# Kernel tuning notes

Hardware: AMD Instinct MI355X
Metric: run time of the kernel (lower is better)

## Reference

```python
import jax, jax.numpy as jnp
import numpy as np

N_NODES = 50000


def _gcn_conv(x, W, b, src, dst, n):
    # PyG GCNConv: h = x @ W, symmetric-normalized aggregation, then + bias.
    h = x @ W  # [N, out]
    deg = jax.ops.segment_sum(jnp.ones_like(dst, dtype=h.dtype), dst, num_segments=n)
    dinv = jnp.where(deg > 0, jax.lax.rsqrt(jnp.maximum(deg, 1e-12)), 0.0)
    norm = dinv[src] * dinv[dst]  # [E]
    msg = h[src] * norm[:, None]  # gather + scale, [E, out]
    out = jax.ops.segment_sum(msg, dst, num_segments=n)
    return out + b


def setup_inputs() -> dict:
    key = jax.random.key(0)
    ks = jax.random.split(key, 8)
    d_in, d_h, d_out = 256, 256, 128
    E = 800000
    x = jax.random.normal(ks[0], (N_NODES, d_in), dtype=jnp.float32)
    edge_index = jax.random.randint(ks[1], (2, E), 0, N_NODES, dtype=jnp.int64)
    def glorot(k, shape):
        lim = np.sqrt(6.0 / (shape[0] + shape[1]))
        return jax.random.uniform(k, shape, jnp.float32, -lim, lim)
    return {
        "x": x,
        "edge_index": edge_index,
        "W1": glorot(ks[2], (d_in, d_h)), "b1": jnp.zeros((d_h,), jnp.float32),
        "W2": glorot(ks[3], (d_h, d_h)), "b2": jnp.zeros((d_h,), jnp.float32),
        "W3": glorot(ks[4], (d_h, d_out)), "b3": jnp.zeros((d_out,), jnp.float32),
    }


def reference(x, edge_index, W1, b1, W2, b2, W3, b3):
    n = x.shape[0]
    # add self-loops once (PyG GCNConv default add_self_loops=True)
    loop = jnp.arange(n, dtype=edge_index.dtype)
    src = jnp.concatenate([edge_index[0], loop])
    dst = jnp.concatenate([edge_index[1], loop])
    h = _gcn_conv(x, W1, b1, src, dst, n)
    h = jax.nn.relu(h)  # dropout is identity in eval mode
    h = _gcn_conv(h, W2, b2, src, dst, n)
    h = jax.nn.relu(h)
    h = _gcn_conv(h, W3, b3, src, dst, n)
    return h
```

## Files before the change

### kernel.cpp

```cpp
#include <hip/hip_runtime.h>
#include <stdint.h>

typedef short v8s __attribute__((ext_vector_type(8)));
typedef float v4f __attribute__((ext_vector_type(4)));
typedef float v2f __attribute__((ext_vector_type(2)));

__device__ inline float bf2f(unsigned short h) {
    union { unsigned u; float f; } c; c.u = ((unsigned)h) << 16; return c.f;
}
__device__ inline unsigned short f2bf(float f) {
    union { float f; unsigned u; } c; c.f = f;
    unsigned u = c.u;
    unsigned r = (u + 0x7FFFu + ((u >> 16) & 1u)) >> 16;
    return (unsigned short)r;
}
__device__ inline void gl_lds16(const unsigned short* g, unsigned short* l) {
    __builtin_amdgcn_global_load_lds(
        (const __attribute__((address_space(1))) unsigned int*)(g),
        (__attribute__((address_space(3))) unsigned int*)(l), 16, 0, 0);
}

__global__ void k_pre1(const int* __restrict__ dst, int E,
                       int* __restrict__ cnt, int* __restrict__ seq,
                       const float* __restrict__ x, unsigned short* __restrict__ A,
                       int n, int mpad,
                       const float* __restrict__ W1, const float* __restrict__ W2,
                       const float* __restrict__ W3, unsigned short* __restrict__ Wt,
                       int gE, int gX) {
    int b = blockIdx.x;
    if (b < gE) {
        int e = b * 256 + threadIdx.x;
        if (e < E) seq[e] = atomicAdd(&cnt[dst[e]], 1);
    } else if (b < gE + gX) {
        int g = (b - gE) * 256 + threadIdx.x;
        int total = mpad * 64;
        if (g >= total) return;
        int row = g >> 6;
        float4 v;
        if (row < n) v = ((const float4*)x)[(size_t)g];
        else v = make_float4(0.f, 0.f, 0.f, 0.f);
        ushort4 o;
        o.x = f2bf(v.x); o.y = f2bf(v.y); o.z = f2bf(v.z); o.w = f2bf(v.w);
        ((ushort4*)A)[(size_t)g] = o;
    } else {
        int idx = (b - gE - gX) * 256 + threadIdx.x;
        const float* W; int base, N;
        if (idx < 65536)       { W = W1; base = 0;      N = 256; }
        else if (idx < 131072) { W = W2; base = 65536;  N = 256; }
        else                   { W = W3; base = 131072; N = 128; }
        int loc = idx - base;
        int nn = loc >> 8;
        int k = loc & 255;
        Wt[idx] = f2bf(W[(size_t)k * N + nn]);
    }
}

__global__ void k_scan1(const int* __restrict__ cnt, int n, int* __restrict__ incl,
                        int* __restrict__ bsum) {
    __shared__ int sm[256];
    int t = threadIdx.x;
    int i = blockIdx.x * 256 + t;
    int v = (i < n) ? cnt[i] : 0;
    sm[t] = v; __syncthreads();
    for (int off = 1; off < 256; off <<= 1) {
        int add = (t >= off) ? sm[t - off] : 0;
        __syncthreads();
        sm[t] += add;
        __syncthreads();
    }
    if (i < n) incl[i] = sm[t];
    if (t == 255) bsum[blockIdx.x] = sm[255];
}

__global__ void k_scan2(const int* __restrict__ bsum, int nb, int* __restrict__ boff) {
    __shared__ int sm[256];
    int t = threadIdx.x;
    int v = (t < nb) ? bsum[t] : 0;
    sm[t] = v; __syncthreads();
    for (int off = 1; off < 256; off <<= 1) {
        int add = (t >= off) ? sm[t - off] : 0;
        __syncthreads();
        sm[t] += add;
        __syncthreads();
    }
    if (t < nb) boff[t] = sm[t] - v;
}

__global__ void k_scan3(const int* __restrict__ cnt, int n, const int* __restrict__ boff,
                        int* __restrict__ rs, float* __restrict__ dinv) {
    int i = blockIdx.x * 256 + threadIdx.x;
    if (i < n) {
        int c = cnt[i];
        rs[i] = rs[i] + boff[blockIdx.x] - c;
        dinv[i] = rsqrtf((float)(c + 1));
    }
}

__global__ void k_scatter2(const int* __restrict__ src, const int* __restrict__ dst,
                           const int* __restrict__ seq, int E,
                           const int* __restrict__ rs, int* __restrict__ col) {
    int e = blockIdx.x * 256 + threadIdx.x;
    if (e < E) col[rs[dst[e]] + seq[e]] = src[e];
}

__launch_bounds__(256, 4)
__global__ void k_gemm(const unsigned short* __restrict__ A,
                       const unsigned short* __restrict__ Wt,
                       unsigned short* __restrict__ Hs,
                       const float* __restrict__ dinv, int n, int N) {
    __shared__ unsigned short sA[128 * 32];
    __shared__ unsigned short sB[128 * 32];
    const int t = threadIdx.x;
    const int lane = t & 63;
    const int wave = t >> 6;
    const int wm = wave >> 1, wn = wave & 1;
    const int m0 = blockIdx.x * 128;
    const int n0 = blockIdx.y * 128;

    v4f acc[4][4];
#pragma unroll
    for (int i = 0; i < 4; i++)
#pragma unroll
        for (int j = 0; j < 4; j++)
#pragma unroll
            for (int r = 0; r < 4; r++) acc[i][j][r] = 0.f;

    const int c0 = t, c1 = t + 256;
    const int r0 = c0 >> 2, kc0 = (c0 & 3) * 8;
    const int r1 = c1 >> 2, kc1 = (c1 & 3) * 8;
    const size_t aBase0 = (size_t)(m0 + r0) * 256 + kc0;
    const size_t aBase1 = (size_t)(m0 + r1) * 256 + kc1;
    const size_t bBase0 = (size_t)(n0 + r0) * 256 + kc0;
    const size_t bBase1 = (size_t)(n0 + r1) * 256 + kc1;

    const int q = lane >> 4;
    const int lm = lane & 15;

    for (int k0 = 0; k0 < 256; k0 += 32) {
        __syncthreads();
        gl_lds16(A + aBase0 + k0, &sA[c0 * 8]);
        gl_lds16(A + aBase1 + k0, &sA[c1 * 8]);
        gl_lds16(Wt + bBase0 + k0, &sB[c0 * 8]);
        gl_lds16(Wt + bBase1 + k0, &sB[c1 * 8]);
        __syncthreads();

        v8s afr[4], bfr[4];
#pragma unroll
        for (int i = 0; i < 4; i++) {
            int r = wm * 64 + i * 16 + lm;
            afr[i] = *(const v8s*)&sA[r * 32 + q * 8];
        }
#pragma unroll
        for (int j = 0; j < 4; j++) {
            int nn = wn * 64 + j * 16 + lm;
            bfr[j] = *(const v8s*)&sB[nn * 32 + q * 8];
        }
#pragma unroll
        for (int i = 0; i < 4; i++)
#pragma unroll
            for (int j = 0; j < 4; j++)
                acc[i][j] = __builtin_amdgcn_mfma_f32_16x16x32_bf16(afr[i], bfr[j],
                                                                    acc[i][j], 0, 0, 0);
    }

#pragma unroll
    for (int i = 0; i < 4; i++) {
        int mbase = m0 + wm * 64 + i * 16 + q * 4;
#pragma unroll
        for (int r = 0; r < 4; r++) {
            int m = mbase + r;
            float s = (m < n) ? dinv[m] : 0.f;
#pragma unroll
            for (int j = 0; j < 4; j++) {
                int colI = n0 + wn * 64 + j * 16 + lm;
                Hs[(size_t)m * N + colI] = f2bf(acc[i][j][r] * s);
            }
        }
    }
}

template <int D, bool RELU, bool F32OUT>
__launch_bounds__(256, 8)
__global__ void k_agg(const unsigned short* __restrict__ Hs,
                      const int* __restrict__ rs, const int* __restrict__ cnt,
                      const int* __restrict__ col, const float* __restrict__ dinv,
                      const float* __restrict__ bias,
                      unsigned short* __restrict__ outb, float* __restrict__ outf,
                      int n, int nzero) {
    constexpr int LPN = D / 8;
    constexpr int NPG = 64 / LPN;
    const int lane = threadIdx.x & 63;
    const int i = blockIdx.x * 4 + (threadIdx.x >> 6);
    if (i >= n) return;
    const int g = lane / LPN;
    const int cl = lane % LPN;

    v2f acc[4];
#pragma unroll
    for (int k = 0; k < 4; k++) acc[k] = (v2f){0.f, 0.f};

    auto accq = [&](unsigned u, int k) {
        union { unsigned uu; float f; } lo, hi;
        lo.uu = u << 16;
        hi.uu = u & 0xffff0000u;
        v2f t; t[0] = lo.f; t[1] = hi.f;
        acc[k] += t;
    };
    auto acc16 = [&](uint4 q) { accq(q.x, 0); accq(q.y, 1); accq(q.z, 2); accq(q.w, 3); };

    const unsigned short* base = Hs + cl * 8;
    const int s = rs[i], deg = cnt[i];
    const int T = deg + 1;
    const int Tpad = (T + NPG - 1) & ~(NPG - 1);

    for (int b = 0; b < Tpad; b += 64) {
        int t = b + lane;
        int v;
        if (t == 0) v = i;
        else if (t <= deg) v = col[s + t - 1];
        else v = nzero;
        int lim = min(64, Tpad - b);
        int t2 = 0;
        for (; t2 + 4 * NPG <= lim; t2 += 4 * NPG) {
            int c0 = __shfl(v, t2 + 0 * NPG + g);
            int c1 = __shfl(v, t2 + 1 * NPG + g);
            int c2 = __shfl(v, t2 + 2 * NPG + g);
            int c3 = __shfl(v, t2 + 3 * NPG + g);
            uint4 q0 = *(const uint4*)(base + (size_t)c0 * D);
            uint4 q1 = *(const uint4*)(base + (size_t)c1 * D);
            uint4 q2 = *(const uint4*)(base + (size_t)c2 * D);
            uint4 q3 = *(const uint4*)(base + (size_t)c3 * D);
            acc16(q0); acc16(q1); acc16(q2); acc16(q3);
        }
        for (; t2 + NPG <= lim; t2 += NPG) {
            int c0 = __shfl(v, t2 + g);
            uint4 q0 = *(const uint4*)(base + (size_t)c0 * D);
            acc16(q0);
        }
    }

#pragma unroll
    for (int off = LPN; off < 64; off <<= 1) {
#pragma unroll
        for (int k = 0; k < 4; k++) {
            acc[k][0] += __shfl_xor(acc[k][0], off);
            acc[k][1] += __shfl_xor(acc[k][1], off);
        }
    }

    if (g == 0) {
        float di = dinv[i];
        float o[8];
#pragma unroll
        for (int k = 0; k < 4; k++) {
            o[2 * k + 0] = di * acc[k][0] + bias[cl * 8 + 2 * k + 0];
            o[2 * k + 1] = di * acc[k][1] + bias[cl * 8 + 2 * k + 1];
        }
        if (RELU) {
#pragma unroll
            for (int k = 0; k < 8; k++) o[k] = fmaxf(o[k], 0.f);
        }
        if constexpr (F32OUT) {
            float* p = outf + (size_t)i * D + cl * 8;
            *(float4*)p = make_float4(o[0], o[1], o[2], o[3]);
            *(float4*)(p + 4) = make_float4(o[4], o[5], o[6], o[7]);
        } else {
            uint4 q;
            q.x = ((unsigned)f2bf(o[1]) << 16) | f2bf(o[0]);
            q.y = ((unsigned)f2bf(o[3]) << 16) | f2bf(o[2]);
            q.z = ((unsigned)f2bf(o[5]) << 16) | f2bf(o[4]);
            q.w = ((unsigned)f2bf(o[7]) << 16) | f2bf(o[6]);
            *(uint4*)(outb + (size_t)i * D + cl * 8) = q;
        }
    }
}

extern "C" void kernel_launch(void* const* d_in, const int* in_sizes, int n_in,
                              void* d_out, int out_size, void* d_ws, size_t ws_size,
                              hipStream_t stream) {
    const float* x  = (const float*)d_in[0];
    const int*   ei = (const int*)d_in[1];
    const float* W1 = (const float*)d_in[2];
    const float* b1 = (const float*)d_in[3];
    const float* W2 = (const float*)d_in[4];
    const float* b2 = (const float*)d_in[5];
    const float* W3 = (const float*)d_in[6];
    const float* b3 = (const float*)d_in[7];

    const int n = in_sizes[0] / 256;
    const int E = in_sizes[1] / 2;
    const int mpad = ((n + 127) / 128) * 128;

    char* ws = (char*)d_ws;
    size_t off = 0;
    auto alloc = [&](size_t bytes) -> void* {
        void* p = ws + off;
        off += (bytes + 255) & ~(size_t)255;
        return p;
    };
    int* cnt      = (int*)alloc((size_t)n * 4);
    int* rs       = (int*)alloc((size_t)n * 4);
    float* dinv   = (float*)alloc((size_t)n * 4);
    int* bsum     = (int*)alloc(256 * 4);
    int* boff     = (int*)alloc(256 * 4);
    int* seq      = (int*)alloc((size_t)E * 4);
    int* col      = (int*)alloc((size_t)E * 4);
    unsigned short* Wt = (unsigned short*)alloc((size_t)163840 * 2);
    unsigned short* W1t = Wt;
    unsigned short* W2t = Wt + 65536;
    unsigned short* W3t = Wt + 131072;
    unsigned short* bufA = (unsigned short*)alloc((size_t)mpad * 256 * 2);
    unsigned short* bufB = (unsigned short*)alloc((size_t)mpad * 256 * 2);
    (void)ws_size; (void)n_in; (void)out_size;

    const int* srcp = ei;
    const int* dstp = ei + E;
    const int gE = (E + 255) / 256;
    const int gN = (n + 255) / 256;
    const int gX = (mpad * 64 + 255) / 256;
    const int gW = 640;

    hipMemsetAsync(cnt, 0, (size_t)n * 4, stream);

    k_pre1<<<gE + gX + gW, 256, 0, stream>>>(dstp, E, cnt, seq, x, bufA, n, mpad,
                                             W1, W2, W3, Wt, gE, gX);
    k_scan1<<<gN, 256, 0, stream>>>(cnt, n, rs, bsum);
    k_scan2<<<1, 256, 0, stream>>>(bsum, gN, boff);
    k_scan3<<<gN, 256, 0, stream>>>(cnt, n, boff, rs, dinv);
    k_scatter2<<<gE, 256, 0, stream>>>(srcp, dstp, seq, E, rs, col);

    const int gAgg = (n + 3) / 4;
    dim3 gg1(mpad / 128, 2);
    k_gemm<<<gg1, 256, 0, stream>>>(bufA, W1t, bufB, dinv, n, 256);
    k_agg<256, true, false><<<gAgg, 256, 0, stream>>>(bufB, rs, cnt, col, dinv, b1,
                                                      bufA, nullptr, n, n);
    k_gemm<<<gg1, 256, 0, stream>>>(bufA, W2t, bufB, dinv, n, 256);
    k_agg<256, true, false><<<gAgg, 256, 0, stream>>>(bufB, rs, cnt, col, dinv, b2,
                                                      bufA, nullptr, n, n);
    dim3 gg3(mpad / 128, 1);
    k_gemm<<<gg3, 256, 0, stream>>>(bufA, W3t, bufB, dinv, n, 128);
    k_agg<128, false, true><<<gAgg, 256, 0, stream>>>(bufB, rs, cnt, col, dinv, b3,
                                                      nullptr, (float*)d_out, n, n);
}
```

Baseline: 354.9 us.

## Double-buffer GEMM LDS tiles and fuse scan stages two and three

The GEMM now keeps two LDS buffers per operand and prefetches the next K-slice while MFMAs run on the current one, with a single barrier per iteration instead of two. Launch bounds drop from 4 to 3 blocks per CU to allow for the doubled shared memory. Separately, the single-block block-offset scan and the apply kernel are merged: each block sums the preceding block totals itself, which removes one launch. Correctness of the one-barrier double buffer depends on the async global-to-LDS loads being complete before the next barrier, and the reduced occupancy could offset some of the overlap gain.

```diff
diff --git a/kernel.cpp b/kernel.cpp
--- a/kernel.cpp
+++ b/kernel.cpp
@@ -72,26 +72,23 @@
     if (t == 255) bsum[blockIdx.x] = sm[255];
 }
 
-__global__ void k_scan2(const int* __restrict__ bsum, int nb, int* __restrict__ boff) {
-    __shared__ int sm[256];
+__global__ void k_scan23(const int* __restrict__ cnt, int n,
+                         const int* __restrict__ bsum,
+                         int* __restrict__ rs, float* __restrict__ dinv) {
+    __shared__ int red[256];
     int t = threadIdx.x;
-    int v = (t < nb) ? bsum[t] : 0;
-    sm[t] = v; __syncthreads();
-    for (int off = 1; off < 256; off <<= 1) {
-        int add = (t >= off) ? sm[t - off] : 0;
+    int acc = 0;
+    for (int j = t; j < (int)blockIdx.x; j += 256) acc += bsum[j];
+    red[t] = acc; __syncthreads();
+    for (int s = 128; s > 0; s >>= 1) {
+        if (t < s) red[t] += red[t + s];
         __syncthreads();
-        sm[t] += add;
-        __syncthreads();
-    }
-    if (t < nb) boff[t] = sm[t] - v;
-}
-
-__global__ void k_scan3(const int* __restrict__ cnt, int n, const int* __restrict__ boff,
-                        int* __restrict__ rs, float* __restrict__ dinv) {
-    int i = blockIdx.x * 256 + threadIdx.x;
+    }
+    int boff = red[0];
+    int i = blockIdx.x * 256 + t;
     if (i < n) {
         int c = cnt[i];
-        rs[i] = rs[i] + boff[blockIdx.x] - c;
+        rs[i] = rs[i] + boff - c;
         dinv[i] = rsqrtf((float)(c + 1));
     }
 }
@@ -103,13 +100,13 @@
     if (e < E) col[rs[dst[e]] + seq[e]] = src[e];
 }
 
-__launch_bounds__(256, 4)
+__launch_bounds__(256, 3)
 __global__ void k_gemm(const unsigned short* __restrict__ A,
                        const unsigned short* __restrict__ Wt,
                        unsigned short* __restrict__ Hs,
                        const float* __restrict__ dinv, int n, int N) {
-    __shared__ unsigned short sA[128 * 32];
-    __shared__ unsigned short sB[128 * 32];
+    __shared__ unsigned short sA[2][128 * 32];
+    __shared__ unsigned short sB[2][128 * 32];
     const int t = threadIdx.x;
     const int lane = t & 63;
     const int wave = t >> 6;
@@ -136,24 +133,32 @@
     const int q = lane >> 4;
     const int lm = lane & 15;
 
+    gl_lds16(A + aBase0, &sA[0][c0 * 8]);
+    gl_lds16(A + aBase1, &sA[0][c1 * 8]);
+    gl_lds16(Wt + bBase0, &sB[0][c0 * 8]);
+    gl_lds16(Wt + bBase1, &sB[0][c1 * 8]);
+
     for (int k0 = 0; k0 < 256; k0 += 32) {
+        const int cur = (k0 >> 5) & 1;
         __syncthreads();
-        gl_lds16(A + aBase0 + k0, &sA[c0 * 8]);
-        gl_lds16(A + aBase1 + k0, &sA[c1 * 8]);
-        gl_lds16(Wt + bBase0 + k0, &sB[c0 * 8]);
-        gl_lds16(Wt + bBase1 + k0, &sB[c1 * 8]);
-        __syncthreads();
+        if (k0 < 224) {
+            const int nxt = cur ^ 1;
+            gl_lds16(A + aBase0 + k0 + 32, &sA[nxt][c0 * 8]);
+            gl_lds16(A + aBase1 + k0 + 32, &sA[nxt][c1 * 8]);
+            gl_lds16(Wt + bBase0 + k0 + 32, &sB[nxt][c0 * 8]);
+            gl_lds16(Wt + bBase1 + k0 + 32, &sB[nxt][c1 * 8]);
+        }
 
         v8s afr[4], bfr[4];
 #pragma unroll
         for (int i = 0; i < 4; i++) {
             int r = wm * 64 + i * 16 + lm;
-            afr[i] = *(const v8s*)&sA[r * 32 + q * 8];
+            afr[i] = *(const v8s*)&sA[cur][r * 32 + q * 8];
         }
 #pragma unroll
         for (int j = 0; j < 4; j++) {
             int nn = wn * 64 + j * 16 + lm;
-            bfr[j] = *(const v8s*)&sB[nn * 32 + q * 8];
+            bfr[j] = *(const v8s*)&sB[cur][nn * 32 + q * 8];
         }
 #pragma unroll
         for (int i = 0; i < 4; i++)
@@ -302,7 +307,6 @@
     int* rs       = (int*)alloc((size_t)n * 4);
     float* dinv   = (float*)alloc((size_t)n * 4);
     int* bsum     = (int*)alloc(256 * 4);
-    int* boff     = (int*)alloc(256 * 4);
     int* seq      = (int*)alloc((size_t)E * 4);
     int* col      = (int*)alloc((size_t)E * 4);
     unsigned short* Wt = (unsigned short*)alloc((size_t)163840 * 2);
@@ -325,8 +329,7 @@
     k_pre1<<<gE + gX + gW, 256, 0, stream>>>(dstp, E, cnt, seq, x, bufA, n, mpad,
                                              W1, W2, W3, Wt, gE, gX);
     k_scan1<<<gN, 256, 0, stream>>>(cnt, n, rs, bsum);
-    k_scan2<<<1, 256, 0, stream>>>(bsum, gN, boff);
-    k_scan3<<<gN, 256, 0, stream>>>(cnt, n, boff, rs, dinv);
+    k_scan23<<<gN, 256, 0, stream>>>(cnt, n, bsum, rs, dinv);
     k_scatter2<<<gE, 256, 0, stream>>>(srcp, dstp, seq, E, rs, col);
 
     const int gAgg = (n + 3) / 4;
```

Result: slower. 364.3 us (+2.6%).

## Merge scan into one kernel and fuse edge scatter with first GEMM launch

Applied to the files above, without the earlier changes.

Replaces the three-kernel prefix scan with a single kernel in which each block recomputes its prefix by reducing all preceding counts. The CSR column scatter is merged into the first GEMM launch as extra blocks, so the two independent pieces of work run concurrently. Together this removes three kernel launches and their serialization gaps. In exchange, each scan block redundantly reads up to n counts, which is quadratic-ish work but small at this size, and the scatter blocks share a launch with the GEMM's register and LDS budget.

```diff
diff --git a/kernel.cpp b/kernel.cpp
--- a/kernel.cpp
+++ b/kernel.cpp
@@ -55,52 +55,108 @@
     }
 }
 
-__global__ void k_scan1(const int* __restrict__ cnt, int n, int* __restrict__ incl,
-                        int* __restrict__ bsum) {
+__global__ void k_scan(const int* __restrict__ cnt, int n,
+                       int* __restrict__ rs, float* __restrict__ dinv) {
     __shared__ int sm[256];
-    int t = threadIdx.x;
-    int i = blockIdx.x * 256 + t;
-    int v = (i < n) ? cnt[i] : 0;
+    __shared__ int preS;
+    const int t = threadIdx.x;
+    const int base = blockIdx.x * 256;
+
+    int acc = 0;
+    for (int j = t; j < base; j += 256) acc += cnt[j];
+    sm[t] = acc; __syncthreads();
+    for (int s = 128; s > 0; s >>= 1) {
+        if (t < s) sm[t] += sm[t + s];
+        __syncthreads();
+    }
+    if (t == 0) preS = sm[0];
+    __syncthreads();
+
+    const int i = base + t;
+    const int v = (i < n) ? cnt[i] : 0;
     sm[t] = v; __syncthreads();
     for (int off = 1; off < 256; off <<= 1) {
-        int add = (t >= off) ? sm[t - off] : 0;
-        __syncthreads();
-        sm[t] += add;
-        __syncthreads();
-    }
-    if (i < n) incl[i] = sm[t];
-    if (t == 255) bsum[blockIdx.x] = sm[255];
-}
-
-__global__ void k_scan2(const int* __restrict__ bsum, int nb, int* __restrict__ boff) {
-    __shared__ int sm[256];
-    int t = threadIdx.x;
-    int v = (t < nb) ? bsum[t] : 0;
-    sm[t] = v; __syncthreads();
-    for (int off = 1; off < 256; off <<= 1) {
-        int add = (t >= off) ? sm[t - off] : 0;
-        __syncthreads();
-        sm[t] += add;
-        __syncthreads();
-    }
-    if (t < nb) boff[t] = sm[t] - v;
-}
-
-__global__ void k_scan3(const int* __restrict__ cnt, int n, const int* __restrict__ boff,
-                        int* __restrict__ rs, float* __restrict__ dinv) {
-    int i = blockIdx.x * 256 + threadIdx.x;
+        int a = (t >= off) ? sm[t - off] : 0;
+        __syncthreads();
+        sm[t] += a;
+        __syncthreads();
+    }
     if (i < n) {
-        int c = cnt[i];
-        rs[i] = rs[i] + boff[blockIdx.x] - c;
-        dinv[i] = rsqrtf((float)(c + 1));
-    }
-}
-
-__global__ void k_scatter2(const int* __restrict__ src, const int* __restrict__ dst,
-                           const int* __restrict__ seq, int E,
-                           const int* __restrict__ rs, int* __restrict__ col) {
-    int e = blockIdx.x * 256 + threadIdx.x;
-    if (e < E) col[rs[dst[e]] + seq[e]] = src[e];
+        rs[i] = preS + sm[t] - v;
+        dinv[i] = rsqrtf((float)(v + 1));
+    }
+}
+
+__device__ __forceinline__ void gemm_body(
+        const unsigned short* __restrict__ A, const unsigned short* __restrict__ Wt,
+        unsigned short* __restrict__ Hs, const float* __restrict__ dinv,
+        int n, int N, int m0, int n0,
+        unsigned short* sA, unsigned short* sB) {
+    const int t = threadIdx.x;
+    const int lane = t & 63;
+    const int wave = t >> 6;
+    const int wm = wave >> 1, wn = wave & 1;
+
+    v4f acc[4][4];
+#pragma unroll
+    for (int i = 0; i < 4; i++)
+#pragma unroll
+        for (int j = 0; j < 4; j++)
+#pragma unroll
+            for (int r = 0; r < 4; r++) acc[i][j][r] = 0.f;
+
+    const int c0 = t, c1 = t + 256;
+    const int r0 = c0 >> 2, kc0 = (c0 & 3) * 8;
+    const int r1 = c1 >> 2, kc1 = (c1 & 3) * 8;
+    const size_t aBase0 = (size_t)(m0 + r0) * 256 + kc0;
+    const size_t aBase1 = (size_t)(m0 + r1) * 256 + kc1;
+    const size_t bBase0 = (size_t)(n0 + r0) * 256 + kc0;
+    const size_t bBase1 = (size_t)(n0 + r1) * 256 + kc1;
+
+    const int q = lane >> 4;
+    const int lm = lane & 15;
+
+    for (int k0 = 0; k0 < 256; k0 += 32) {
+        __syncthreads();
+        gl_lds16(A + aBase0 + k0, &sA[c0 * 8]);
+        gl_lds16(A + aBase1 + k0, &sA[c1 * 8]);
+        gl_lds16(Wt + bBase0 + k0, &sB[c0 * 8]);
+        gl_lds16(Wt + bBase1 + k0, &sB[c1 * 8]);
+        __syncthreads();
+
+        v8s afr[4], bfr[4];
+#pragma unroll
+        for (int i = 0; i < 4; i++) {
+            int r = wm * 64 + i * 16 + lm;
+            afr[i] = *(const v8s*)&sA[r * 32 + q * 8];
+        }
+#pragma unroll
+        for (int j = 0; j < 4; j++) {
+            int nn = wn * 64 + j * 16 + lm;
+            bfr[j] = *(const v8s*)&sB[nn * 32 + q * 8];
+        }
+#pragma unroll
+        for (int i = 0; i < 4; i++)
+#pragma unroll
+            for (int j = 0; j < 4; j++)
+                acc[i][j] = __builtin_amdgcn_mfma_f32_16x16x32_bf16(afr[i], bfr[j],
+                                                                    acc[i][j], 0, 0, 0);
+    }
+
+#pragma unroll
+    for (int i = 0; i < 4; i++) {
+        int mbase = m0 + wm * 64 + i * 16 + q * 4;
+#pragma unroll
+        for (int r = 0; r < 4; r++) {
+            int m = mbase + r;
+            float s = (m < n) ? dinv[m] : 0.f;
+#pragma unroll
+            for (int j = 0; j < 4; j++) {
+                int colI = n0 + wn * 64 + j * 16 + lm;
+                Hs[(size_t)m * N + colI] = f2bf(acc[i][j][r] * s);
+            }
+        }
+    }
 }
 
 __launch_bounds__(256, 4)
@@ -110,73 +166,28 @@
                        const float* __restrict__ dinv, int n, int N) {
     __shared__ unsigned short sA[128 * 32];
     __shared__ unsigned short sB[128 * 32];
-    const int t = threadIdx.x;
-    const int lane = t & 63;
-    const int wave = t >> 6;
-    const int wm = wave >> 1, wn = wave & 1;
-    const int m0 = blockIdx.x * 128;
-    const int n0 = blockIdx.y * 128;
-
-    v4f acc[4][4];
-#pragma unroll
-    for (int i = 0; i < 4; i++)
-#pragma unroll
-        for (int j = 0; j < 4; j++)
-#pragma unroll
-            for (int r = 0; r < 4; r++) acc[i][j][r] = 0.f;
-
-    const int c0 = t, c1 = t + 256;
-    const int r0 = c0 >> 2, kc0 = (c0 & 3) * 8;
-    const int r1 = c1 >> 2, kc1 = (c1 & 3) * 8;
-    const size_t aBase0 = (size_t)(m0 + r0) * 256 + kc0;
-    const size_t aBase1 = (size_t)(m0 + r1) * 256 + kc1;
-    const size_t bBase0 = (size_t)(n0 + r0) * 256 + kc0;
-    const size_t bBase1 = (size_t)(n0 + r1) * 256 + kc1;
-
-    const int q = lane >> 4;
-    const int lm = lane & 15;
-
-    for (int k0 = 0; k0 < 256; k0 += 32) {
-        __syncthreads();
-        gl_lds16(A + aBase0 + k0, &sA[c0 * 8]);
-        gl_lds16(A + aBase1 + k0, &sA[c1 * 8]);
-        gl_lds16(Wt + bBase0 + k0, &sB[c0 * 8]);
-        gl_lds16(Wt + bBase1 + k0, &sB[c1 * 8]);
-        __syncthreads();
-
-        v8s afr[4], bfr[4];
-#pragma unroll
-        for (int i = 0; i < 4; i++) {
-            int r = wm * 64 + i * 16 + lm;
-            afr[i] = *(const v8s*)&sA[r * 32 + q * 8];
-        }
-#pragma unroll
-        for (int j = 0; j < 4; j++) {
-            int nn = wn * 64 + j * 16 + lm;
-            bfr[j] = *(const v8s*)&sB[nn * 32 + q * 8];
-        }
-#pragma unroll
-        for (int i = 0; i < 4; i++)
-#pragma unroll
-            for (int j = 0; j < 4; j++)
-                acc[i][j] = __builtin_amdgcn_mfma_f32_16x16x32_bf16(afr[i], bfr[j],
-                                                                    acc[i][j], 0, 0, 0);
-    }
-
-#pragma unroll
-    for (int i = 0; i < 4; i++) {
-        int mbase = m0 + wm * 64 + i * 16 + q * 4;
-#pragma unroll
-        for (int r = 0; r < 4; r++) {
-            int m = mbase + r;
-            float s = (m < n) ? dinv[m] : 0.f;
-#pragma unroll
-            for (int j = 0; j < 4; j++) {
-                int colI = n0 + wn * 64 + j * 16 + lm;
-                Hs[(size_t)m * N + colI] = f2bf(acc[i][j][r] * s);
-            }
-        }
-    }
+    gemm_body(A, Wt, Hs, dinv, n, N, blockIdx.x * 128, blockIdx.y * 128, sA, sB);
+}
+
+__launch_bounds__(256, 4)
+__global__ void k_sg(const unsigned short* __restrict__ A,
+                     const unsigned short* __restrict__ Wt,
+                     unsigned short* __restrict__ Hs,
+                     const float* __restrict__ dinv, int n, int N, int nmb,
+                     const int* __restrict__ src, const int* __restrict__ dst,
+                     const int* __restrict__ seq, int E,
+                     const int* __restrict__ rs, int* __restrict__ col,
+                     int gemmBlocks) {
+    __shared__ unsigned short sA[128 * 32];
+    __shared__ unsigned short sB[128 * 32];
+    const int b = blockIdx.x;
+    if (b >= gemmBlocks) {
+        int e = (b - gemmBlocks) * 256 + threadIdx.x;
+        if (e < E) col[rs[dst[e]] + seq[e]] = src[e];
+        return;
+    }
+    const int bx = b % nmb, by = b / nmb;
+    gemm_body(A, Wt, Hs, dinv, n, N, bx * 128, by * 128, sA, sB);
 }
 
 template <int D, bool RELU, bool F32OUT>
@@ -295,14 +306,12 @@
     size_t off = 0;
     auto alloc = [&](size_t bytes) -> void* {
         void* p = ws + off;
-        off += (bytes + 255) & ~(size_t)255;
+        off += (bytes + 511) & ~(size_t)511;
         return p;
     };
     int* cnt      = (int*)alloc((size_t)n * 4);
     int* rs       = (int*)alloc((size_t)n * 4);
     float* dinv   = (float*)alloc((size_t)n * 4);
-    int* bsum     = (int*)alloc(256 * 4);
-    int* boff     = (int*)alloc(256 * 4);
     int* seq      = (int*)alloc((size_t)E * 4);
     int* col      = (int*)alloc((size_t)E * 4);
     unsigned short* Wt = (unsigned short*)alloc((size_t)163840 * 2);
@@ -319,25 +328,26 @@
     const int gN = (n + 255) / 256;
     const int gX = (mpad * 64 + 255) / 256;
     const int gW = 640;
+    const int nmb = mpad / 128;
 
     hipMemsetAsync(cnt, 0, (size_t)n * 4, stream);
 
     k_pre1<<<gE + gX + gW, 256, 0, stream>>>(dstp, E, cnt, seq, x, bufA, n, mpad,
                                              W1, W2, W3, Wt, gE, gX);
-    k_scan1<<<gN, 256, 0, stream>>>(cnt, n, rs, bsum);
-    k_scan2<<<1, 256, 0, stream>>>(bsum, gN, boff);
-    k_scan3<<<gN, 256, 0, stream>>>(cnt, n, boff, rs, dinv);
-    k_scatter2<<<gE, 256, 0, stream>>>(srcp, dstp, seq, E, rs, col);
+    k_scan<<<gN, 256, 0, stream>>>(cnt, n, rs, dinv);
+
+    const int gemmBlocks = nmb * 2;
+    k_sg<<<gemmBlocks + gE, 256, 0, stream>>>(bufA, W1t, bufB, dinv, n, 256, nmb,
+                                              srcp, dstp, seq, E, rs, col, gemmBlocks);
 
     const int gAgg = (n + 3) / 4;
-    dim3 gg1(mpad / 128, 2);
-    k_gemm<<<gg1, 256, 0, stream>>>(bufA, W1t, bufB, dinv, n, 256);
     k_agg<256, true, false><<<gAgg, 256, 0, stream>>>(bufB, rs, cnt, col, dinv, b1,
                                                       bufA, nullptr, n, n);
-    k_gemm<<<gg1, 256, 0, stream>>>(bufA, W2t, bufB, dinv, n, 256);
+    dim3 gg2(nmb, 2);
+    k_gemm<<<gg2, 256, 0, stream>>>(bufA, W2t, bufB, dinv, n, 256);
     k_agg<256, true, false><<<gAgg, 256, 0, stream>>>(bufB, rs, cnt, col, dinv, b2,
                                                       bufA, nullptr, n, n);
-    dim3 gg3(mpad / 128, 1);
+    dim3 gg3(nmb, 1);
     k_gemm<<<gg3, 256, 0, stream>>>(bufA, W3t, bufB, dinv, n, 128);
     k_agg<128, false, true><<<gAgg, 256, 0, stream>>>(bufB, rs, cnt, col, dinv, b3,
                                                       nullptr, (float*)d_out, n, n);
```

After: 381.2 us. 1.07x slower.

## Fuse x bf16 conversion into first GEMM and merge scan kernels

Applied to the files above, without the earlier changes.

Removes the separate fp32-to-bf16 conversion of x from the preprocessing kernel and adds a k_gemm_x variant that loads fp32 x directly, converts in registers and writes into LDS, so the bf16 copy of x is never written or re-read. It also fuses the block-offset scan and finalize kernels into one, where each block reduces the preceding block sums itself, saving one launch. In exchange, the first GEMM uses plain register loads instead of direct global-to-LDS loads and reads x once per column tile (twice in total). The pre-kernel is no longer slowed by the conversion work.

```diff
diff --git a/kernel.cpp b/kernel.cpp
--- a/kernel.cpp
+++ b/kernel.cpp
@@ -22,28 +22,15 @@
 
 __global__ void k_pre1(const int* __restrict__ dst, int E,
                        int* __restrict__ cnt, int* __restrict__ seq,
-                       const float* __restrict__ x, unsigned short* __restrict__ A,
-                       int n, int mpad,
                        const float* __restrict__ W1, const float* __restrict__ W2,
                        const float* __restrict__ W3, unsigned short* __restrict__ Wt,
-                       int gE, int gX) {
+                       int gE) {
     int b = blockIdx.x;
     if (b < gE) {
         int e = b * 256 + threadIdx.x;
         if (e < E) seq[e] = atomicAdd(&cnt[dst[e]], 1);
-    } else if (b < gE + gX) {
-        int g = (b - gE) * 256 + threadIdx.x;
-        int total = mpad * 64;
-        if (g >= total) return;
-        int row = g >> 6;
-        float4 v;
-        if (row < n) v = ((const float4*)x)[(size_t)g];
-        else v = make_float4(0.f, 0.f, 0.f, 0.f);
-        ushort4 o;
-        o.x = f2bf(v.x); o.y = f2bf(v.y); o.z = f2bf(v.z); o.w = f2bf(v.w);
-        ((ushort4*)A)[(size_t)g] = o;
     } else {
-        int idx = (b - gE - gX) * 256 + threadIdx.x;
+        int idx = (b - gE) * 256 + threadIdx.x;
         const float* W; int base, N;
         if (idx < 65536)       { W = W1; base = 0;      N = 256; }
         else if (idx < 131072) { W = W2; base = 65536;  N = 256; }
@@ -72,26 +59,23 @@
     if (t == 255) bsum[blockIdx.x] = sm[255];
 }
 
-__global__ void k_scan2(const int* __restrict__ bsum, int nb, int* __restrict__ boff) {
-    __shared__ int sm[256];
+__global__ void k_scan23(const int* __restrict__ cnt, int n,
+                         const int* __restrict__ bsum,
+                         int* __restrict__ rs, float* __restrict__ dinv) {
+    __shared__ int red[256];
     int t = threadIdx.x;
-    int v = (t < nb) ? bsum[t] : 0;
-    sm[t] = v; __syncthreads();
-    for (int off = 1; off < 256; off <<= 1) {
-        int add = (t >= off) ? sm[t - off] : 0;
-        __syncthreads();
-        sm[t] += add;
-        __syncthreads();
-    }
-    if (t < nb) boff[t] = sm[t] - v;
-}
-
-__global__ void k_scan3(const int* __restrict__ cnt, int n, const int* __restrict__ boff,
-                        int* __restrict__ rs, float* __restrict__ dinv) {
-    int i = blockIdx.x * 256 + threadIdx.x;
+    int acc = 0;
+    for (int j = t; j < (int)blockIdx.x; j += 256) acc += bsum[j];
+    red[t] = acc; __syncthreads();
+    for (int s = 128; s > 0; s >>= 1) {
+        if (t < s) red[t] += red[t + s];
+        __syncthreads();
+    }
+    int boff = red[0];
+    int i = blockIdx.x * 256 + t;
     if (i < n) {
         int c = cnt[i];
-        rs[i] = rs[i] + boff[blockIdx.x] - c;
+        rs[i] = rs[i] + boff - c;
         dinv[i] = rsqrtf((float)(c + 1));
     }
 }
@@ -142,6 +126,97 @@
         gl_lds16(A + aBase1 + k0, &sA[c1 * 8]);
         gl_lds16(Wt + bBase0 + k0, &sB[c0 * 8]);
         gl_lds16(Wt + bBase1 + k0, &sB[c1 * 8]);
+        __syncthreads();
+
+        v8s afr[4], bfr[4];
+#pragma unroll
+        for (int i = 0; i < 4; i++) {
+            int r = wm * 64 + i * 16 + lm;
+            afr[i] = *(const v8s*)&sA[r * 32 + q * 8];
+        }
+#pragma unroll
+        for (int j = 0; j < 4; j++) {
+            int nn = wn * 64 + j * 16 + lm;
+            bfr[j] = *(const v8s*)&sB[nn * 32 + q * 8];
+        }
+#pragma unroll
+        for (int i = 0; i < 4; i++)
+#pragma unroll
+            for (int j = 0; j < 4; j++)
+                acc[i][j] = __builtin_amdgcn_mfma_f32_16x16x32_bf16(afr[i], bfr[j],
+                                                                    acc[i][j], 0, 0, 0);
+    }
+
+#pragma unroll
+    for (int i = 0; i < 4; i++) {
+        int mbase = m0 + wm * 64 + i * 16 + q * 4;
+#pragma unroll
+        for (int r = 0; r < 4; r++) {
+            int m = mbase + r;
+            float s = (m < n) ? dinv[m] : 0.f;
+#pragma unroll
+            for (int j = 0; j < 4; j++) {
+                int colI = n0 + wn * 64 + j * 16 + lm;
+                Hs[(size_t)m * N + colI] = f2bf(acc[i][j][r] * s);
+            }
+        }
+    }
+}
+
+__launch_bounds__(256, 4)
+__global__ void k_gemm_x(const float* __restrict__ x,
+                         const unsigned short* __restrict__ Wt,
+                         unsigned short* __restrict__ Hs,
+                         const float* __restrict__ dinv, int n, int N) {
+    __shared__ unsigned short sA[128 * 32];
+    __shared__ unsigned short sB[128 * 32];
+    const int t = threadIdx.x;
+    const int lane = t & 63;
+    const int wave = t >> 6;
+    const int wm = wave >> 1, wn = wave & 1;
+    const int m0 = blockIdx.x * 128;
+    const int n0 = blockIdx.y * 128;
+
+    v4f acc[4][4];
+#pragma unroll
+    for (int i = 0; i < 4; i++)
+#pragma unroll
+        for (int j = 0; j < 4; j++)
+#pragma unroll
+            for (int r = 0; r < 4; r++) acc[i][j][r] = 0.f;
+
+    const int c0 = t, c1 = t + 256;
+    const int r0 = c0 >> 2, kc0 = (c0 & 3) * 8;
+    const int r1 = c1 >> 2, kc1 = (c1 & 3) * 8;
+    const int ra0 = min(m0 + r0, n - 1);
+    const int ra1 = min(m0 + r1, n - 1);
+    const float* ax0 = x + (size_t)ra0 * 256 + kc0;
+    const float* ax1 = x + (size_t)ra1 * 256 + kc1;
+    const size_t bBase0 = (size_t)(n0 + r0) * 256 + kc0;
+    const size_t bBase1 = (size_t)(n0 + r1) * 256 + kc1;
+
+    const int q = lane >> 4;
+    const int lm = lane & 15;
+
+    for (int k0 = 0; k0 < 256; k0 += 32) {
+        __syncthreads();
+        float4 u0 = *(const float4*)(ax0 + k0);
+        float4 u1 = *(const float4*)(ax0 + k0 + 4);
+        float4 u2 = *(const float4*)(ax1 + k0);
+        float4 u3 = *(const float4*)(ax1 + k0 + 4);
+        gl_lds16(Wt + bBase0 + k0, &sB[c0 * 8]);
+        gl_lds16(Wt + bBase1 + k0, &sB[c1 * 8]);
+        v8s w0, w1;
+        w0[0] = (short)f2bf(u0.x); w0[1] = (short)f2bf(u0.y);
+        w0[2] = (short)f2bf(u0.z); w0[3] = (short)f2bf(u0.w);
+        w0[4] = (short)f2bf(u1.x); w0[5] = (short)f2bf(u1.y);
+        w0[6] = (short)f2bf(u1.z); w0[7] = (short)f2bf(u1.w);
+        w1[0] = (short)f2bf(u2.x); w1[1] = (short)f2bf(u2.y);
+        w1[2] = (short)f2bf(u2.z); w1[3] = (short)f2bf(u2.w);
+        w1[4] = (short)f2bf(u3.x); w1[5] = (short)f2bf(u3.y);
+        w1[6] = (short)f2bf(u3.z); w1[7] = (short)f2bf(u3.w);
+        *(v8s*)&sA[c0 * 8] = w0;
+        *(v8s*)&sA[c1 * 8] = w1;
         __syncthreads();
 
         v8s afr[4], bfr[4];
@@ -302,7 +377,6 @@
     int* rs       = (int*)alloc((size_t)n * 4);
     float* dinv   = (float*)alloc((size_t)n * 4);
     int* bsum     = (int*)alloc(256 * 4);
-    int* boff     = (int*)alloc(256 * 4);
     int* seq      = (int*)alloc((size_t)E * 4);
     int* col      = (int*)alloc((size_t)E * 4);
     unsigned short* Wt = (unsigned short*)alloc((size_t)163840 * 2);
@@ -317,27 +391,25 @@
     const int* dstp = ei + E;
     const int gE = (E + 255) / 256;
     const int gN = (n + 255) / 256;
-    const int gX = (mpad * 64 + 255) / 256;
     const int gW = 640;
+    const int nmb = mpad / 128;
 
     hipMemsetAsync(cnt, 0, (size_t)n * 4, stream);
 
-    k_pre1<<<gE + gX + gW, 256, 0, stream>>>(dstp, E, cnt, seq, x, bufA, n, mpad,
-                                             W1, W2, W3, Wt, gE, gX);
+    k_pre1<<<gE + gW, 256, 0, stream>>>(dstp, E, cnt, seq, W1, W2, W3, Wt, gE);
     k_scan1<<<gN, 256, 0, stream>>>(cnt, n, rs, bsum);
-    k_scan2<<<1, 256, 0, stream>>>(bsum, gN, boff);
-    k_scan3<<<gN, 256, 0, stream>>>(cnt, n, boff, rs, dinv);
+    k_scan23<<<gN, 256, 0, stream>>>(cnt, n, bsum, rs, dinv);
     k_scatter2<<<gE, 256, 0, stream>>>(srcp, dstp, seq, E, rs, col);
 
     const int gAgg = (n + 3) / 4;
-    dim3 gg1(mpad / 128, 2);
-    k_gemm<<<gg1, 256, 0, stream>>>(bufA, W1t, bufB, dinv, n, 256);
+    dim3 gg1(nmb, 2);
+    k_gemm_x<<<gg1, 256, 0, stream>>>(x, W1t, bufB, dinv, n, 256);
     k_agg<256, true, false><<<gAgg, 256, 0, stream>>>(bufB, rs, cnt, col, dinv, b1,
                                                       bufA, nullptr, n, n);
     k_gemm<<<gg1, 256, 0, stream>>>(bufA, W2t, bufB, dinv, n, 256);
     k_agg<256, true, false><<<gAgg, 256, 0, stream>>>(bufB, rs, cnt, col, dinv, b2,
                                                       bufA, nullptr, n, n);
-    dim3 gg3(mpad / 128, 1);
+    dim3 gg3(nmb, 1);
     k_gemm<<<gg3, 256, 0, stream>>>(bufA, W3t, bufB, dinv, n, 128);
     k_agg<128, false, true><<<gAgg, 256, 0, stream>>>(bufB, rs, cnt, col, dinv, b3,
                                                       nullptr, (float*)d_out, n, n);
```

Result: no change. 356.1 us (+0.3%).
